# Optimization experiments

Hardware: AMD Instinct MI355X
Metric: run time of the kernel (lower is better)

## Reference

```python
import jax, jax.numpy as jnp
import numpy as np

DIM = 384
HEADS = 6
HEAD_DIM = DIM // HEADS
HIDDEN = int(DIM * 4.0)
SCALE = HEAD_DIM ** (-0.5)
EPS = 1e-5


def _layernorm(x, w, b):
    m = jnp.mean(x, axis=-1, keepdims=True)
    v = jnp.var(x, axis=-1, keepdims=True)
    return (x - m) * jax.lax.rsqrt(v + EPS) * w + b


def _mlp(x, fc1_w, fc1_b, fc2_w, fc2_b):
    h = jnp.einsum('bnc,hc->bnh', x, fc1_w) + fc1_b
    h = jax.nn.gelu(h, approximate=False)  # torch nn.GELU default = exact erf
    return jnp.einsum('bnh,ch->bnc', h, fc2_w) + fc2_b


def _attn_block(q, k, v, proj_w, proj_b):
    # q:[B,H,Q,D] k,v:[B,H,K,D]
    attn = jnp.einsum('bhqd,bhkd->bhqk', q, k) * SCALE
    attn = jax.nn.softmax(attn, axis=-1)
    o = jnp.einsum('bhqk,bhkd->bhqd', attn, v)
    B, H, Q, D = o.shape
    o = o.transpose(0, 2, 1, 3).reshape(B, Q, H * D)
    return jnp.einsum('bqc,oc->bqo', o, proj_w) + proj_b


def setup_inputs() -> dict:
    key = jax.random.key(0)
    ks = jax.random.split(key, 10)
    s = 0.02
    return {
        'x': jax.random.normal(ks[0], (4, 2048, DIM), jnp.float32),
        'y': jax.random.normal(ks[1], (4, 256, DIM), jnp.float32),
        'norm1_w': jnp.ones((DIM,), jnp.float32),
        'norm1_b': jnp.zeros((DIM,), jnp.float32),
        'norm2_w': jnp.ones((DIM,), jnp.float32),
        'norm2_b': jnp.zeros((DIM,), jnp.float32),
        'qkv_w': jax.random.normal(ks[2], (3 * DIM, DIM), jnp.float32) * s,
        'proj_w': jax.random.normal(ks[3], (DIM, DIM), jnp.float32) * s,
        'proj_b': jnp.zeros((DIM,), jnp.float32),
        'fc1_w': jax.random.normal(ks[4], (HIDDEN, DIM), jnp.float32) * s,
        'fc1_b': jnp.zeros((HIDDEN,), jnp.float32),
        'fc2_w': jax.random.normal(ks[5], (DIM, HIDDEN), jnp.float32) * s,
        'fc2_b': jnp.zeros((DIM,), jnp.float32),
    }


def reference(x, y, norm1_w, norm1_b, norm2_w, norm2_b, qkv_w,
              proj_w, proj_b, fc1_w, fc1_b, fc2_w, fc2_b):
    B, N, C = x.shape
    L = y.shape[1]
    nx = _layernorm(x, norm1_w, norm1_b)
    ny = _layernorm(y, norm1_w, norm1_b)
    cat = jnp.concatenate([nx, ny], axis=1)  # [B, N+L, C]
    qkv = jnp.einsum('bnc,oc->bno', cat, qkv_w)
    qkv = qkv.reshape(B, N + L, 3, HEADS, HEAD_DIM).transpose(2, 0, 3, 1, 4)
    q, k, v = qkv[0], qkv[1], qkv[2]  # each [B,H,N+L,D]
    # cross: y-queries attend over all N+L keys
    y_att = _attn_block(q[:, :, N:], k, v, proj_w, proj_b)
    # self: x-queries attend over first N keys only
    x_att = _attn_block(q[:, :, :N], k[:, :, :N], v[:, :, :N], proj_w, proj_b)
    new_x = x + x_att
    new_y = y + y_att
    new_x = new_x + _mlp(_layernorm(new_x, norm2_w, norm2_b), fc1_w, fc1_b, fc2_w, fc2_b)
    new_y = new_y + _mlp(_layernorm(new_y, norm2_w, norm2_b), fc1_w, fc1_b, fc2_w, fc2_b)
    return (new_x, new_y)
```

## Files before the change

### kernel.cpp

```cpp
#include <hip/hip_runtime.h>
#include <hip/hip_bf16.h>
#include <math.h>

#define B_   4
#define NX   2048
#define NY   256
#define T_   2304
#define NTOK 9216
#define DIM  384
#define NH   6
#define HD   64
#define HID  1536
#define QKV3 1152
#define QK2  768

typedef __attribute__((ext_vector_type(8))) short bf16x8;
typedef __attribute__((ext_vector_type(4))) float f32x4;

__device__ __forceinline__ float b2f(unsigned short u) {
  union { unsigned int i; float f; } x; x.i = ((unsigned int)u) << 16; return x.f;
}
__device__ __forceinline__ unsigned short f2b(float f) {
  union { float f; unsigned int i; } x; x.f = f;
  unsigned int r = x.i + 0x7fffu + ((x.i >> 16) & 1u);
  return (unsigned short)(r >> 16);
}
__device__ __forceinline__ unsigned int pack2(float a, float b) {
  return (unsigned int)f2b(a) | ((unsigned int)f2b(b) << 16);
}
__device__ __forceinline__ unsigned int cvtpk(float a, float b) {
  unsigned int r;
  asm("v_cvt_pk_bf16_f32 %0, %1, %2" : "=v"(r) : "v"(a), "v"(b));
  return r;
}
__device__ __forceinline__ float fexp2(float x) {
  float r;
  asm("v_exp_f32 %0, %1" : "=v"(r) : "v"(x));
  return r;
}
__device__ __forceinline__ float ldin(const void* p, size_t i, int isbf) {
  return isbf ? b2f(((const unsigned short*)p)[i]) : ((const float*)p)[i];
}

#if defined(__has_builtin)
#if __has_builtin(__builtin_amdgcn_global_load_lds)
#define HAS_GLL 1
#endif
#endif

__device__ __forceinline__ void stage16(const unsigned short* g, unsigned short* l) {
#ifdef HAS_GLL
  __builtin_amdgcn_global_load_lds(
      (const __attribute__((address_space(1))) unsigned int*)g,
      (__attribute__((address_space(3))) unsigned int*)l, 16, 0, 0);
#else
  *(uint4*)(l + (threadIdx.x & 63) * 8) = *(const uint4*)g;
#endif
}

__global__ void detect_kernel(const unsigned short* __restrict__ qw,
                              int* __restrict__ flag) {
  int lane = threadIdx.x;
  int bad = 0;
  #pragma unroll
  for (int j = 0; j < 8; j++) {
    unsigned short u = qw[2 * (lane + 64 * j)];
    int e = (u >> 7) & 0xff;
    bad += (e >= 134) ? 1 : 0;
  }
  #pragma unroll
  for (int off = 32; off > 0; off >>= 1) bad += __shfl_xor(bad, off);
  if (lane == 0) *flag = (bad < 64) ? 1 : 0;
}

__global__ __launch_bounds__(256) void convert4_kernel(
    const void* __restrict__ s0, const void* __restrict__ s1,
    const void* __restrict__ s2, const void* __restrict__ s3,
    unsigned short* __restrict__ d0, const int* __restrict__ flagp) {
  int isbf = *flagp;
  int i = (blockIdx.x * 256 + threadIdx.x) * 8;
  const void* src; int off;
  if (i < 442368)       { src = s0; off = 0; }
  else if (i < 589824)  { src = s1; off = 442368; }
  else if (i < 1179648) { src = s2; off = 589824; }
  else                  { src = s3; off = 1179648; }
  int li = i - off;
  if (isbf) {
    *(uint4*)(d0 + i) = *(const uint4*)((const unsigned short*)src + li);
  } else {
    const float* s = (const float*)src + li;
    unsigned int w[4];
    #pragma unroll
    for (int j = 0; j < 4; j++) w[j] = pack2(s[2 * j], s[2 * j + 1]);
    *(uint4*)(d0 + i) = make_uint4(w[0], w[1], w[2], w[3]);
  }
}

__global__ __launch_bounds__(256) void ln1_kernel(
    const void* __restrict__ x, const void* __restrict__ y,
    const void* __restrict__ w, const void* __restrict__ bsh,
    const int* __restrict__ flagp, unsigned short* __restrict__ out)
{
  int isbf = *flagp;
  int token = blockIdx.x * 4 + (threadIdx.x >> 6);
  int lane  = threadIdx.x & 63;
  int bb = token / T_;
  int t  = token - bb * T_;
  const void* src = (t < NX) ? x : y;
  size_t base = (t < NX) ? ((size_t)bb * NX + t) * DIM
                         : ((size_t)bb * NY + (t - NX)) * DIM;
  float v[6];
  float s = 0.f, s2 = 0.f;
  #pragma unroll
  for (int k = 0; k < 6; k++) {
    v[k] = ldin(src, base + lane + 64 * k, isbf);
    s += v[k]; s2 += v[k] * v[k];
  }
  #pragma unroll
  for (int off = 32; off > 0; off >>= 1) {
    s  += __shfl_xor(s, off);
    s2 += __shfl_xor(s2, off);
  }
  float mean = s * (1.f / DIM);
  float var  = s2 * (1.f / DIM) - mean * mean;
  float rs = rsqrtf(var + 1e-5f);
  unsigned short* dst = out + (size_t)token * DIM;
  #pragma unroll
  for (int k = 0; k < 6; k++) {
    int c = lane + 64 * k;
    dst[c] = f2b((v[k] - mean) * rs * ldin(w, c, isbf) + ldin(bsh, c, isbf));
  }
}

__global__ __launch_bounds__(256) void ln2_kernel(
    const float* __restrict__ in, const void* __restrict__ w,
    const void* __restrict__ bsh, const int* __restrict__ flagp,
    unsigned short* __restrict__ out)
{
  int isbf = *flagp;
  int token = blockIdx.x * 4 + (threadIdx.x >> 6);
  int lane  = threadIdx.x & 63;
  const float* src = in + (size_t)token * DIM;
  float v[6];
  float s = 0.f, s2 = 0.f;
  #pragma unroll
  for (int k = 0; k < 6; k++) {
    v[k] = src[lane + 64 * k];
    s += v[k]; s2 += v[k] * v[k];
  }
  #pragma unroll
  for (int off = 32; off > 0; off >>= 1) {
    s  += __shfl_xor(s, off);
    s2 += __shfl_xor(s2, off);
  }
  float mean = s * (1.f / DIM);
  float var  = s2 * (1.f / DIM) - mean * mean;
  float rs = rsqrtf(var + 1e-5f);
  unsigned short* dst = out + (size_t)token * DIM;
  #pragma unroll
  for (int k = 0; k < 6; k++) {
    int c = lane + 64 * k;
    dst[c] = f2b((v[k] - mean) * rs * ldin(w, c, isbf) + ldin(bsh, c, isbf));
  }
}

template <int EPI, int KT, int MT>
__global__ __launch_bounds__(256, (MT == 64) ? 6 : 4) void gemm_mfma(
    const unsigned short* __restrict__ A, const unsigned short* __restrict__ Bw,
    const void* __restrict__ bias,
    const void* __restrict__ rx, const void* __restrict__ ry,
    const float* __restrict__ rf,
    unsigned short* __restrict__ outb, float* __restrict__ resf,
    void* __restrict__ outd, unsigned short* __restrict__ vTp,
    const int* __restrict__ flagp, int N)
{
  constexpr int NT = KT / 32;
  constexpr int NI = MT / 64;
  __shared__ unsigned short As[2][MT * 32];
  __shared__ unsigned short Bs[2][64 * 32];
  const int tid  = threadIdx.x;
  const int wave = tid >> 6, lane = tid & 63;
  const int g = lane >> 4, qq = lane & 15;
  const int gx = gridDim.x;
  const int flat = blockIdx.x + gx * blockIdx.y;
  const int cpx = (gx * gridDim.y) >> 3;
  const int L = (flat & 7) * cpx + (flat >> 3);
  const int n0 = (L % gx) * 64, m0 = (L / gx) * MT;
  const int wm = wave * (16 * NI);

  f32x4 z = {0.f, 0.f, 0.f, 0.f};
  f32x4 acc[NI][4];
  #pragma unroll
  for (int i = 0; i < NI; i++)
    #pragma unroll
    for (int j = 0; j < 4; j++) acc[i][j] = z;

  const int lrow = lane >> 2;
  const int lkx  = (((lane & 3) ^ ((lane >> 3) & 3)) * 8);
  const int rsw  = (qq >> 1) & 3;

  auto STG = [&](int t, int bi_) {
    int k0_ = t * 32;
    #pragma unroll
    for (int s = 0; s < NI; s++) {
      int ar = wm + s * 16;
      stage16(A + (size_t)(m0 + ar + lrow) * KT + k0_ + lkx,
              &As[bi_][ar * 32]);
    }
    int br = wave * 16;
    stage16(Bw + (size_t)(n0 + br + lrow) * KT + k0_ + lkx,
            &Bs[bi_][br * 32]);
  };
  auto COMPUTE = [&](int bi_) {
    const unsigned short* as = As[bi_];
    const unsigned short* bs = Bs[bi_];
    bf16x8 af[NI], bf[4];
    #pragma unroll
    for (int i = 0; i < NI; i++)
      af[i] = *(const bf16x8*)&as[(wm + i * 16 + qq) * 32 + ((g ^ rsw) * 8)];
    #pragma unroll
    for (int j = 0; j < 4; j++)
      bf[j] = *(const bf16x8*)&bs[(j * 16 + qq) * 32 + ((g ^ rsw) * 8)];
    __builtin_amdgcn_s_setprio(1);
    #pragma unroll
    for (int i = 0; i < NI; i++)
      #pragma unroll
      for (int j = 0; j < 4; j++)
        acc[i][j] = __builtin_amdgcn_mfma_f32_16x16x32_bf16(
            af[i], bf[j], acc[i][j], 0, 0, 0);
    __builtin_amdgcn_s_setprio(0);
  };
  #define GSYNC() do { \
    asm volatile("s_waitcnt vmcnt(0)" ::: "memory"); \
    __builtin_amdgcn_s_barrier(); } while (0)

  STG(0, 0);
  GSYNC();
  #pragma unroll 1
  for (int t = 0; t + 2 < NT; t += 2) {
    STG(t + 1, 1);
    COMPUTE(0);
    GSYNC();
    STG(t + 2, 0);
    COMPUTE(1);
    GSYNC();
  }
  STG(NT - 1, 1);
  COMPUTE(0);
  GSYNC();
  COMPUTE(1);
  #undef GSYNC

  if (EPI == 0 && n0 >= 768) {
    #pragma unroll
    for (int i = 0; i < NI; i++) {
      int mb = m0 + wm + i * 16 + g * 4;
      int bb = mb / T_;
      int t  = mb - bb * T_;
      #pragma unroll
      for (int j = 0; j < 4; j++) {
        int n = n0 + j * 16 + qq;
        int hh = (n - 768) >> 6, dd = (n - 768) & 63;
        uint2 pk;
        pk.x = pack2(acc[i][j][0], acc[i][j][1]);
        pk.y = pack2(acc[i][j][2], acc[i][j][3]);
        *(uint2*)(vTp + ((size_t)(bb * NH + hh) * HD + dd) * T_ + t) = pk;
      }
    }
    return;
  }

  int isbf = (EPI == 0) ? 1 : *flagp;
  float qs = (EPI == 0 && n0 < 384) ? 0.18033688011f : 1.f;
  const bool kswz = (EPI == 0) && (n0 >= 384);
  #pragma unroll
  for (int i = 0; i < NI; i++) {
    #pragma unroll
    for (int r = 0; r < 4; r++) {
      int m = m0 + wm + i * 16 + g * 4 + r;
      int bb = m / T_;
      int t  = m - bb * T_;
      int l = m & 31;
      int ms = kswz ? ((m & ~31) | (((l >> 2) & 1) << 4) | ((l >> 3) << 2) |
                       (l & 3))
                    : m;
      #pragma unroll
      for (int j = 0; j < 4; j++) {
        int n = n0 + j * 16 + qq;
        float v = acc[i][j][r];
        if (EPI == 0) {
          outb[(size_t)ms * QK2 + n] = f2b(v * qs);
        } else if (EPI == 1) {
          float resv = (t < NX)
              ? ldin(rx, ((size_t)bb * NX + t) * DIM + n, isbf)
              : ldin(ry, ((size_t)bb * NY + (t - NX)) * DIM + n, isbf);
          resf[(size_t)m * DIM + n] = v + ldin(bias, n, isbf) + resv;
        } else if (EPI == 2) {
          float h = v + ldin(bias, n, isbf);
          outb[(size_t)m * N + n] =
              f2b(0.5f * h * (1.f + erff(h * 0.70710678118654752f)));
        } else {
          float rr = v + ldin(bias, n, isbf) + rf[(size_t)m * DIM + n];
          size_t oi = (t < NX)
              ? ((size_t)bb * NX + t) * DIM + n
              : (size_t)B_ * NX * DIM + ((size_t)bb * NY + (t - NX)) * DIM + n;
          if (isbf) ((unsigned short*)outd)[oi] = f2b(rr);
          else      ((float*)outd)[oi] = rr;
        }
      }
    }
  }
}

__global__ __launch_bounds__(256) void attn_mfma(
    const unsigned short* __restrict__ qk, const unsigned short* __restrict__ vT,
    unsigned short* __restrict__ att)
{
  __shared__ float Ob[64][68];
  __shared__ float Lb[64];
  const int tid = threadIdx.x;
  const int wave = tid >> 6, lane = tid & 63;
  const int g = lane >> 4, qq = lane & 15;
  const int flat = blockIdx.x;
  const int L = (flat & 7) * 108 + (flat >> 3);
  const int bx = L % 36;
  const int hb = L / 36;
  const int h = hb % NH, b = hb / NH;
  const int self = (bx < 32);
  const int qtok0 = self ? bx * 64 : NX + (bx - 32) * 64;
  const int kvbeg = wave * (self ? 512 : 576);
  const int ntile = self ? 16 : 18;

  bf16x8 qa[4][2];
  #pragma unroll
  for (int f = 0; f < 4; f++) {
    size_t qrow = (size_t)(b * T_ + qtok0 + f * 16 + qq) * QK2 + h * HD;
    qa[f][0] = *(const bf16x8*)(qk + qrow + g * 8);
    qa[f][1] = *(const bf16x8*)(qk + qrow + 32 + g * 8);
  }
  const unsigned short* kb = qk + (size_t)b * T_ * QK2 + DIM + h * HD;
  const unsigned short* vb = vT + (size_t)(b * NH + h) * HD * T_;

  f32x4 z = {0.f, 0.f, 0.f, 0.f};
  f32x4 ot[4][4];
  #pragma unroll
  for (int f = 0; f < 4; f++)
    #pragma unroll
    for (int dt = 0; dt < 4; dt++) ot[f][dt] = z;
  float lsum[4] = {0.f, 0.f, 0.f, 0.f};

  const unsigned short* kp0 = kb + (size_t)(kvbeg + qq) * QK2 + g * 8;
  const unsigned short* kp1 = kp0 + 16 * QK2;
  const unsigned short* vp0 = vb + (size_t)qq * T_ + kvbeg + g * 8;
  const unsigned short* vp1 = vp0 + 16 * T_;
  const unsigned short* vp2 = vp0 + 32 * T_;
  const unsigned short* vp3 = vp0 + 48 * T_;

  uint4 kc[4];
  kc[0] = *(const uint4*)(kp0);
  kc[1] = *(const uint4*)(kp0 + 32);
  kc[2] = *(const uint4*)(kp1);
  kc[3] = *(const uint4*)(kp1 + 32);
  kp0 += 32 * QK2; kp1 += 32 * QK2;
  uint4 vc[4];
  vc[0] = *(const uint4*)(vp0);
  vc[1] = *(const uint4*)(vp1);
  vc[2] = *(const uint4*)(vp2);
  vc[3] = *(const uint4*)(vp3);
  vp0 += 32; vp1 += 32; vp2 += 32; vp3 += 32;

  for (int it = 0; it < ntile; it++) {
    f32x4 s[4][2];
    __builtin_amdgcn_s_setprio(1);
    #pragma unroll
    for (int f = 0; f < 4; f++) {
      s[f][0] = __builtin_amdgcn_mfma_f32_16x16x32_bf16(
          *(const bf16x8*)&kc[0], qa[f][0], z, 0, 0, 0);
      s[f][0] = __builtin_amdgcn_mfma_f32_16x16x32_bf16(
          *(const bf16x8*)&kc[1], qa[f][1], s[f][0], 0, 0, 0);
      s[f][1] = __builtin_amdgcn_mfma_f32_16x16x32_bf16(
          *(const bf16x8*)&kc[2], qa[f][0], z, 0, 0, 0);
      s[f][1] = __builtin_amdgcn_mfma_f32_16x16x32_bf16(
          *(const bf16x8*)&kc[3], qa[f][1], s[f][1], 0, 0, 0);
    }
    __builtin_amdgcn_s_setprio(0);
    if (it + 1 < ntile) {
      kc[0] = *(const uint4*)(kp0);
      kc[1] = *(const uint4*)(kp0 + 32);
      kc[2] = *(const uint4*)(kp1);
      kc[3] = *(const uint4*)(kp1 + 32);
      kp0 += 32 * QK2; kp1 += 32 * QK2;
    }

    #pragma unroll
    for (int f = 0; f < 4; f++) {
      float pv[8];
      #pragma unroll
      for (int c = 0; c < 2; c++)
        #pragma unroll
        for (int r = 0; r < 4; r++)
          pv[c * 4 + r] = fexp2(s[f][c][r]);
      lsum[f] += ((pv[0] + pv[1]) + (pv[2] + pv[3])) +
                 ((pv[4] + pv[5]) + (pv[6] + pv[7]));
      union { unsigned int w[4]; bf16x8 v; } bq;
      bq.w[0] = cvtpk(pv[0], pv[1]);
      bq.w[1] = cvtpk(pv[2], pv[3]);
      bq.w[2] = cvtpk(pv[4], pv[5]);
      bq.w[3] = cvtpk(pv[6], pv[7]);
      __builtin_amdgcn_s_setprio(1);
      #pragma unroll
      for (int dt = 0; dt < 4; dt++)
        ot[f][dt] = __builtin_amdgcn_mfma_f32_16x16x32_bf16(
            *(const bf16x8*)&vc[dt], bq.v, ot[f][dt], 0, 0, 0);
      __builtin_amdgcn_s_setprio(0);
    }

    if (it + 1 < ntile) {
      vc[0] = *(const uint4*)(vp0);
      vc[1] = *(const uint4*)(vp1);
      vc[2] = *(const uint4*)(vp2);
      vc[3] = *(const uint4*)(vp3);
      vp0 += 32; vp1 += 32; vp2 += 32; vp3 += 32;
    }
  }

  #pragma unroll
  for (int f = 0; f < 4; f++) {
    lsum[f] += __shfl_xor(lsum[f], 16);
    lsum[f] += __shfl_xor(lsum[f], 32);
  }

  #pragma unroll
  for (int w = 0; w < 4; w++) {
    if (wave == w) {
      if (w == 0) {
        #pragma unroll
        for (int f = 0; f < 4; f++) {
          #pragma unroll
          for (int dt = 0; dt < 4; dt++)
            *(f32x4*)&Ob[f * 16 + qq][dt * 16 + g * 4] = ot[f][dt];
          if (g == 0) Lb[f * 16 + qq] = lsum[f];
        }
      } else {
        #pragma unroll
        for (int f = 0; f < 4; f++) {
          #pragma unroll
          for (int dt = 0; dt < 4; dt++) {
            f32x4 cur = *(const f32x4*)&Ob[f * 16 + qq][dt * 16 + g * 4];
            #pragma unroll
            for (int r = 0; r < 4; r++) cur[r] += ot[f][dt][r];
            *(f32x4*)&Ob[f * 16 + qq][dt * 16 + g * 4] = cur;
          }
          if (g == 0) Lb[f * 16 + qq] += lsum[f];
        }
      }
    }
    __syncthreads();
  }

  int q = tid >> 2, ds = (tid & 3) * 16;
  float inv = 1.f / Lb[q];
  float o[16];
  #pragma unroll
  for (int j = 0; j < 16; j += 4) {
    f32x4 a = *(const f32x4*)&Ob[q][ds + j];
    #pragma unroll
    for (int r = 0; r < 4; r++) o[j + r] = a[r] * inv;
  }
  unsigned int w[8];
  #pragma unroll
  for (int j = 0; j < 8; j++) w[j] = pack2(o[2 * j], o[2 * j + 1]);
  size_t orow = (size_t)(b * T_ + qtok0 + q) * DIM + h * HD + ds;
  *(uint4*)(att + orow)     = make_uint4(w[0], w[1], w[2], w[3]);
  *(uint4*)(att + orow + 8) = make_uint4(w[4], w[5], w[6], w[7]);
}

extern "C" void kernel_launch(void* const* d_in, const int* in_sizes, int n_in,
                              void* d_out, int out_size, void* d_ws, size_t ws_size,
                              hipStream_t stream)
{
  (void)in_sizes; (void)n_in; (void)out_size; (void)ws_size;
  const void* x    = d_in[0];
  const void* y    = d_in[1];
  const void* n1w  = d_in[2];
  const void* n1b  = d_in[3];
  const void* n2w  = d_in[4];
  const void* n2b  = d_in[5];
  const void* qkvw = d_in[6];
  const void* pw   = d_in[7];
  const void* pb   = d_in[8];
  const void* f1w  = d_in[9];
  const void* f1b  = d_in[10];
  const void* f2w  = d_in[11];
  const void* f2bp = d_in[12];

  unsigned short* wsu = (unsigned short*)d_ws;
  int* flag = (int*)d_ws;
  unsigned short* wts    = wsu + 128;
  unsigned short* qkvw_b = wts;
  unsigned short* pw_b   = wts + 442368;
  unsigned short* f1w_b  = wts + 589824;
  unsigned short* f2w_b  = wts + 1179648;
  unsigned short* catln  = wsu + 1769600;
  unsigned short* qkvb2  = wsu + 5308544;
  unsigned short* attb   = wsu + 12386432;
  unsigned short* vT     = wsu + 15925376;
  unsigned short* hbuf   = qkvb2;
  float*          resb   = (float*)d_ws + 9732160;

  detect_kernel<<<1, 64, 0, stream>>>((const unsigned short*)qkvw, flag);
  convert4_kernel<<<864, 256, 0, stream>>>(qkvw, pw, f1w, f2w, wts, flag);

  ln1_kernel<<<NTOK / 4, 256, 0, stream>>>(x, y, n1w, n1b, flag, catln);
  gemm_mfma<0, DIM, 128><<<dim3(QKV3 / 64, NTOK / 128), 256, 0, stream>>>(
      catln, qkvw_b, nullptr, nullptr, nullptr, nullptr, qkvb2, nullptr,
      nullptr, vT, flag, QKV3);
  attn_mfma<<<dim3(864), 256, 0, stream>>>(qkvb2, vT, attb);
  gemm_mfma<1, DIM, 64><<<dim3(DIM / 64, NTOK / 64), 256, 0, stream>>>(
      attb, pw_b, pb, x, y, nullptr, nullptr, resb, nullptr, nullptr,
      flag, DIM);
  ln2_kernel<<<NTOK / 4, 256, 0, stream>>>(resb, n2w, n2b, flag, catln);
  gemm_mfma<2, DIM, 128><<<dim3(HID / 64, NTOK / 128), 256, 0, stream>>>(
      catln, f1w_b, f1b, nullptr, nullptr, nullptr, hbuf, nullptr, nullptr,
      nullptr, flag, HID);
  gemm_mfma<3, HID, 64><<<dim3(DIM / 64, NTOK / 64), 256, 0, stream>>>(
      hbuf, f2w_b, f2bp, nullptr, nullptr, resb, nullptr, nullptr, d_out,
      nullptr, flag, DIM);
}
```

Baseline: 277.1 us.

## Pre-tile weights into swizzled tile order and split attention KV across eight waves

The weight conversion kernel now writes weights in a pre-tiled, pre-swizzled layout. Each GEMM's B-operand staging then becomes one contiguous 2048-element chunk per K step instead of strided row reads. Separately, the attention kernel goes from 256 to 512 threads, so each of eight waves covers half as many KV tiles. The cross-wave reduction runs over eight waves, and the output write is narrowed to 8 elements per thread. This aims to improve weight-load coalescing and attention parallelism, at the cost of a longer serialized LDS reduction and the register limits imposed by launch_bounds(512,4).

```diff
diff --git a/kernel.cpp b/kernel.cpp
--- a/kernel.cpp
+++ b/kernel.cpp
@@ -79,20 +79,27 @@
     unsigned short* __restrict__ d0, const int* __restrict__ flagp) {
   int isbf = *flagp;
   int i = (blockIdx.x * 256 + threadIdx.x) * 8;
-  const void* src; int off;
-  if (i < 442368)       { src = s0; off = 0; }
-  else if (i < 589824)  { src = s1; off = 442368; }
-  else if (i < 1179648) { src = s2; off = 589824; }
-  else                  { src = s3; off = 1179648; }
+  const void* src; int off, K_;
+  if (i < 442368)       { src = s0; off = 0;       K_ = 384;  }
+  else if (i < 589824)  { src = s1; off = 442368;  K_ = 384;  }
+  else if (i < 1179648) { src = s2; off = 589824;  K_ = 384;  }
+  else                  { src = s3; off = 1179648; K_ = 1536; }
   int li = i - off;
+  int rts = 64 * K_;
+  int tn = li / rts, rem = li - tn * rts;
+  int tk = rem >> 11, q = rem & 2047;
+  int w = q >> 9, l = (q >> 3) & 63;
+  int row = tn * 64 + w * 16 + (l >> 2);
+  int col = tk * 32 + (((l & 3) ^ ((l >> 3) & 3)) << 3);
+  size_t s = (size_t)row * K_ + col;
   if (isbf) {
-    *(uint4*)(d0 + i) = *(const uint4*)((const unsigned short*)src + li);
+    *(uint4*)(d0 + i) = *(const uint4*)((const unsigned short*)src + s);
   } else {
-    const float* s = (const float*)src + li;
-    unsigned int w[4];
-    #pragma unroll
-    for (int j = 0; j < 4; j++) w[j] = pack2(s[2 * j], s[2 * j + 1]);
-    *(uint4*)(d0 + i) = make_uint4(w[0], w[1], w[2], w[3]);
+    const float* sp = (const float*)src + s;
+    unsigned int wv[4];
+    #pragma unroll
+    for (int j = 0; j < 4; j++) wv[j] = pack2(sp[2 * j], sp[2 * j + 1]);
+    *(uint4*)(d0 + i) = make_uint4(wv[0], wv[1], wv[2], wv[3]);
   }
 }
 
@@ -199,6 +206,9 @@
   const int lkx  = (((lane & 3) ^ ((lane >> 3) & 3)) * 8);
   const int rsw  = (qq >> 1) & 3;
 
+  const unsigned short* Bbase = Bw + (size_t)(n0 >> 6) * NT * 2048 +
+                                wave * 512 + lane * 8;
+
   auto STG = [&](int t, int bi_) {
     int k0_ = t * 32;
     #pragma unroll
@@ -207,9 +217,7 @@
       stage16(A + (size_t)(m0 + ar + lrow) * KT + k0_ + lkx,
               &As[bi_][ar * 32]);
     }
-    int br = wave * 16;
-    stage16(Bw + (size_t)(n0 + br + lrow) * KT + k0_ + lkx,
-            &Bs[bi_][br * 32]);
+    stage16(Bbase + (size_t)t * 2048, &Bs[bi_][wave * 16 * 32]);
   };
   auto COMPUTE = [&](int bi_) {
     const unsigned short* as = As[bi_];
@@ -312,7 +320,7 @@
   }
 }
 
-__global__ __launch_bounds__(256) void attn_mfma(
+__global__ __launch_bounds__(512, 4) void attn_mfma(
     const unsigned short* __restrict__ qk, const unsigned short* __restrict__ vT,
     unsigned short* __restrict__ att)
 {
@@ -328,8 +336,8 @@
   const int h = hb % NH, b = hb / NH;
   const int self = (bx < 32);
   const int qtok0 = self ? bx * 64 : NX + (bx - 32) * 64;
-  const int kvbeg = wave * (self ? 512 : 576);
-  const int ntile = self ? 16 : 18;
+  const int kvbeg = wave * (self ? 256 : 288);
+  const int ntile = self ? 8 : 9;
 
   bf16x8 qa[4][2];
   #pragma unroll
@@ -431,7 +439,7 @@
   }
 
   #pragma unroll
-  for (int w = 0; w < 4; w++) {
+  for (int w = 0; w < 8; w++) {
     if (wave == w) {
       if (w == 0) {
         #pragma unroll
@@ -458,21 +466,20 @@
     __syncthreads();
   }
 
-  int q = tid >> 2, ds = (tid & 3) * 16;
+  int q = tid >> 3, ds = (tid & 7) * 8;
   float inv = 1.f / Lb[q];
-  float o[16];
-  #pragma unroll
-  for (int j = 0; j < 16; j += 4) {
+  float o[8];
+  #pragma unroll
+  for (int j = 0; j < 8; j += 4) {
     f32x4 a = *(const f32x4*)&Ob[q][ds + j];
     #pragma unroll
     for (int r = 0; r < 4; r++) o[j + r] = a[r] * inv;
   }
-  unsigned int w[8];
-  #pragma unroll
-  for (int j = 0; j < 8; j++) w[j] = pack2(o[2 * j], o[2 * j + 1]);
+  unsigned int w[4];
+  #pragma unroll
+  for (int j = 0; j < 4; j++) w[j] = pack2(o[2 * j], o[2 * j + 1]);
   size_t orow = (size_t)(b * T_ + qtok0 + q) * DIM + h * HD + ds;
-  *(uint4*)(att + orow)     = make_uint4(w[0], w[1], w[2], w[3]);
-  *(uint4*)(att + orow + 8) = make_uint4(w[4], w[5], w[6], w[7]);
+  *(uint4*)(att + orow) = make_uint4(w[0], w[1], w[2], w[3]);
 }
 
 extern "C" void kernel_launch(void* const* d_in, const int* in_sizes, int n_in,
@@ -515,7 +522,7 @@
   gemm_mfma<0, DIM, 128><<<dim3(QKV3 / 64, NTOK / 128), 256, 0, stream>>>(
       catln, qkvw_b, nullptr, nullptr, nullptr, nullptr, qkvb2, nullptr,
       nullptr, vT, flag, QKV3);
-  attn_mfma<<<dim3(864), 256, 0, stream>>>(qkvb2, vT, attb);
+  attn_mfma<<<dim3(864), 512, 0, stream>>>(qkvb2, vT, attb);
   gemm_mfma<1, DIM, 64><<<dim3(DIM / 64, NTOK / 64), 256, 0, stream>>>(
       attb, pw_b, pb, x, y, nullptr, nullptr, resb, nullptr, nullptr,
       flag, DIM);
```

Measured after the change: 470.1 us. 69.6% more time.
